# Performance work log

Hardware: AMD Instinct MI355X
Metric: run time of the kernel (lower is better)

## Reference

```python
import jax, jax.numpy as jnp
import numpy as np

D_MODEL = 128
NUM_HEADS = 8
DEPTH = D_MODEL // NUM_HEADS
NEG = -1e9


def _dense_params(key, d_in, d_out):
    kw, kb = jax.random.split(key)
    # Glorot-uniform like keras Dense default
    lim = np.sqrt(6.0 / (d_in + d_out))
    w = jax.random.uniform(kw, (d_in, d_out), jnp.float32, -lim, lim)
    b = jnp.zeros((d_out,), jnp.float32)
    return w, b


def setup_inputs() -> dict:
    key = jax.random.key(0)
    ks = jax.random.split(key, 16)
    B, N, M, d = 256, 128, 128, D_MODEL
    inp = {
        'x_self': jax.random.normal(ks[0], (B, N, d), jnp.float32),
        'adj_self': jax.random.randint(ks[1], (B, N, N), 0, 2, jnp.int32),
        'mask_self': jnp.ones((B, N), jnp.int32),
        'x_cross': jax.random.normal(ks[2], (B, M, d), jnp.float32),
        'mask_cross': jnp.ones((B, M), jnp.int32),
    }
    names = ['wq_s', 'wk_s', 'wv_s', 'wo_s', 'wq_c', 'wk_c', 'wv_c', 'wo_c']
    for i, nm in enumerate(names):
        w, b = _dense_params(ks[3 + i], d, d)
        inp[nm] = w
        inp['b' + nm[1:]] = b
    wg, bg = _dense_params(ks[12], 3 * d, d)
    inp['wg'] = wg
    inp['bg'] = bg
    return inp


def _split_heads(x):
    B, N, _ = x.shape
    return x.reshape(B, N, NUM_HEADS, DEPTH).transpose(0, 2, 1, 3)  # [B,H,N,depth]


def _merge_heads(x):
    B, H, N, Dp = x.shape
    return x.transpose(0, 2, 1, 3).reshape(B, N, H * Dp)


def _attention(q, k, v, mask, adj=None):
    # q,k,v: [B,H,Nq,depth]; mask: [B,Nk]; adj: [B,Nq,Nk] or None
    logits = jnp.einsum('bhqd,bhkd->bhqk', q, k) / jnp.sqrt(jnp.float32(DEPTH))
    if adj is not None:
        logits = logits + ((1.0 - adj.astype(jnp.float32)) * NEG)[:, None, :, :]
    logits = logits + ((1.0 - mask.astype(jnp.float32)) * NEG)[:, None, None, :]
    w = jax.nn.softmax(logits, axis=-1)
    return jnp.einsum('bhqk,bhkd->bhqd', w, v)


def reference(x_self, adj_self, mask_self, x_cross, mask_cross,
              wq_s, bq_s, wk_s, bk_s, wv_s, bv_s, wo_s, bo_s,
              wq_c, bq_c, wk_c, bk_c, wv_c, bv_c, wo_c, bo_c,
              wg, bg):
    # Self attention (adjacency + padding mask)
    q_s = _split_heads(x_self @ wq_s + bq_s)
    k_s = _split_heads(x_self @ wk_s + bk_s)
    v_s = _split_heads(x_self @ wv_s + bv_s)
    out_s = _merge_heads(_attention(q_s, k_s, v_s, mask_self, adj_self)) @ wo_s + bo_s
    # Cross attention (padding mask only); dropout inactive at inference
    q_c = _split_heads(x_self @ wq_c + bq_c)
    k_c = _split_heads(x_cross @ wk_c + bk_c)
    v_c = _split_heads(x_cross @ wv_c + bv_c)
    out_c = _merge_heads(_attention(q_c, k_c, v_c, mask_cross)) @ wo_c + bo_c
    # Sigmoid gate fusion
    gate = jax.nn.sigmoid(jnp.concatenate([x_self, out_s, out_c], axis=-1) @ wg + bg)
    return (1.0 - gate) * out_s + gate * out_c
```

## Files before the change

kernel.cpp:

```cpp
#include <hip/hip_runtime.h>
#include <hip/hip_bf16.h>

typedef _Float16 f16_t;
typedef __attribute__((ext_vector_type(8))) _Float16 f16x8;
typedef __attribute__((ext_vector_type(4))) float f32x4;

__device__ __forceinline__ f16x8 cvt8(const float* p) {
  float4 v0 = *(const float4*)p;
  float4 v1 = *(const float4*)(p + 4);
  f16x8 a;
  a[0] = (f16_t)v0.x; a[1] = (f16_t)v0.y; a[2] = (f16_t)v0.z; a[3] = (f16_t)v0.w;
  a[4] = (f16_t)v1.x; a[5] = (f16_t)v1.y; a[6] = (f16_t)v1.z; a[7] = (f16_t)v1.w;
  return a;
}

__global__ __launch_bounds__(256) void prep_kernel(
    const float* wq_s, const float* wk_s, const float* wv_s,
    const float* wq_c, const float* wk_c, const float* wv_c,
    const float* wo_s, const float* wo_c, const float* wg,
    const float* bos, const float* boc, const float* bgin,
    f16_t* WT, float* bgp)
{
  const int b = blockIdx.x;
  const int tid = threadIdx.x;
  if (b < 11) {
    __shared__ float t[128][129];
    const float* src; f16_t* dst; int ostride;
    switch (b) {
      case 0: src = wq_s; break; case 1: src = wk_s; break;
      case 2: src = wv_s; break; case 3: src = wq_c; break;
      case 4: src = wk_c; break; case 5: src = wv_c; break;
      case 6: src = wo_s; break; case 7: src = wo_c; break;
      default: src = wg + (size_t)(b - 8) * 16384; break;
    }
    if (b < 8) { dst = WT + (size_t)b * 16384; ostride = 128; }
    else       { dst = WT + 8 * 16384 + (b - 8) * 128; ostride = 384; }
#pragma unroll
    for (int i = 0; i < 64; ++i) {
      const int idx = tid + i * 256;
      t[idx & 127][idx >> 7] = src[idx];
    }
    __syncthreads();
#pragma unroll
    for (int i = 0; i < 64; ++i) {
      const int idx = tid + i * 256;
      const int c = idx >> 7, r = idx & 127;
      dst[(size_t)c * ostride + r] = (f16_t)t[c][r];
    }
  } else if (b < 13) {
    const int matsel = b - 11;
    const float* wo = matsel ? wo_c : wo_s;
    const int joff = 128 + matsel * 128;
    f16_t* dst = WT + (size_t)(11 + matsel) * 16384;
    const int wv = tid >> 6, ln = tid & 63, l15 = ln & 15, g = ln >> 4;
    f32x4 acc[2][8];
#pragma unroll
    for (int mm = 0; mm < 2; ++mm)
#pragma unroll
      for (int nt = 0; nt < 8; ++nt) acc[mm][nt] = (f32x4){0.f, 0.f, 0.f, 0.f};
#pragma unroll
    for (int kt = 0; kt < 4; ++kt) {
      f16x8 a[2];
#pragma unroll
      for (int mm = 0; mm < 2; ++mm) {
        const int crow = wv * 32 + mm * 16 + l15;
#pragma unroll
        for (int jj = 0; jj < 8; ++jj)
          a[mm][jj] = (f16_t)wg[(size_t)(joff + kt * 32 + g * 8 + jj) * 128 + crow];
      }
#pragma unroll
      for (int nt = 0; nt < 8; ++nt) {
        f16x8 bf = cvt8(wo + (size_t)(nt * 16 + l15) * 128 + kt * 32 + g * 8);
        acc[0][nt] = __builtin_amdgcn_mfma_f32_16x16x32_f16(a[0], bf, acc[0][nt], 0, 0, 0);
        acc[1][nt] = __builtin_amdgcn_mfma_f32_16x16x32_f16(a[1], bf, acc[1][nt], 0, 0, 0);
      }
    }
#pragma unroll
    for (int mm = 0; mm < 2; ++mm)
#pragma unroll
      for (int nt = 0; nt < 8; ++nt)
#pragma unroll
        for (int r = 0; r < 4; ++r) {
          const int c = wv * 32 + mm * 16 + g * 4 + r;
          dst[(size_t)c * 128 + nt * 16 + l15] = (f16_t)acc[mm][nt][r];
        }
  } else {
    if (tid < 128) {
      float acc = bgin[tid];
      for (int j = 0; j < 128; ++j)
        acc += bos[j] * wg[(size_t)(128 + j) * 128 + tid] +
               boc[j] * wg[(size_t)(256 + j) * 128 + tid];
      bgp[tid] = acc;
    }
  }
}

template <bool TRANSP>
__device__ __forceinline__ void gemm_w(
    const f16x8 afr[4], const f16_t* __restrict__ W, const float* __restrict__ bias,
    char* Ob, int l15, int g, int wv)
{
  f32x4 acc[8];
#pragma unroll
  for (int nt = 0; nt < 8; ++nt) acc[nt] = (f32x4){0.f, 0.f, 0.f, 0.f};
#pragma unroll
  for (int nt = 0; nt < 8; ++nt)
#pragma unroll
    for (int kt = 0; kt < 4; ++kt) {
      f16x8 b = *(const f16x8*)(W + (size_t)(nt * 16 + l15) * 128 + kt * 32 + g * 8);
      acc[nt] = __builtin_amdgcn_mfma_f32_16x16x32_f16(afr[kt], b, acc[nt], 0, 0, 0);
    }
#pragma unroll
  for (int nt = 0; nt < 8; ++nt) {
    const int col = nt * 16 + l15;
    const float bv = bias[col];
#pragma unroll
    for (int r = 0; r < 4; ++r) {
      const int row = wv * 16 + g * 4 + r;
      const f16_t v = (f16_t)(acc[nt][r] + bv);
      if (TRANSP)
        *(f16_t*)(Ob + col * 256 + ((row * 2) ^ ((col & 7) << 4))) = v;
      else
        *(f16_t*)(Ob + row * 256 + ((col * 2) ^ ((row & 7) << 4))) = v;
    }
  }
}

__device__ __forceinline__ void attn_wave(
    char* Qb, const char* Kb, const char* Vtb, const unsigned aw[4],
    char* Pw, int l15, int g, int wv)
{
  const int q = wv * 16 + l15;
  const int qsw = (q & 7) << 4;
  const int psw = (l15 & 7) << 4;
  const f32x4 zero = (f32x4){0.f, 0.f, 0.f, 0.f};

#pragma unroll
  for (int h = 0; h < 8; ++h) {
    f16x8 bq = {0, 0, 0, 0, 0, 0, 0, 0};
    if (g < 2) bq = *(const f16x8*)(Qb + q * 256 + ((h * 32 + g * 16) ^ qsw));
    f32x4 st[8];
#pragma unroll
    for (int kt = 0; kt < 8; ++kt) {
      const int krow = kt * 16 + l15;
      f16x8 ak = {0, 0, 0, 0, 0, 0, 0, 0};
      if (g < 2)
        ak = *(const f16x8*)(Kb + krow * 256 + ((h * 32 + g * 16) ^ ((krow & 7) << 4)));
      st[kt] = __builtin_amdgcn_mfma_f32_16x16x32_f16(ak, bq, zero, 0, 0, 0);
    }
    float psum = 0.f;
#pragma unroll
    for (int kt = 0; kt < 8; ++kt)
#pragma unroll
      for (int r = 0; r < 4; ++r) {
        const int k = kt * 16 + g * 4 + r;
        const float e = __expf(st[kt][r] * 0.25f - 8.f);
        const float p = ((aw[kt >> 1] >> (k & 31)) & 1u) ? e : 0.f;
        psum += p;
        st[kt][r] = p;
      }
    psum += __shfl_xor(psum, 16);
    psum += __shfl_xor(psum, 32);
    const float inv = 1.f / psum;

    f32x4 o = zero;
#pragma unroll
    for (int half = 0; half < 2; ++half) {
#pragma unroll
      for (int kt2 = 0; kt2 < 4; ++kt2) {
        const int kt = half * 4 + kt2;
        union { f16_t hh[4]; unsigned long long u; } pk;
#pragma unroll
        for (int r = 0; r < 4; ++r) pk.hh[r] = (f16_t)(st[kt][r] * inv);
        *(unsigned long long*)(Pw + l15 * 128 + ((kt2 * 32 + g * 8) ^ psw)) = pk.u;
      }
#pragma unroll
      for (int kt32 = 0; kt32 < 2; ++kt32) {
        f16x8 pa = *(const f16x8*)(Pw + l15 * 128 + ((kt32 * 64 + g * 16) ^ psw));
        const int d = h * 16 + l15;
        f16x8 vb = *(const f16x8*)(Vtb + d * 256 +
                     (((half * 64 + kt32 * 32 + g * 8) * 2) ^ ((d & 7) << 4)));
        o = __builtin_amdgcn_mfma_f32_16x16x32_f16(pa, vb, o, 0, 0, 0);
      }
    }
#pragma unroll
    for (int r = 0; r < 4; ++r) {
      const int qo = wv * 16 + g * 4 + r;
      *(f16_t*)(Qb + qo * 256 + (((h * 16 + l15) * 2) ^ ((qo & 7) << 4))) = (f16_t)o[r];
    }
  }
}

__global__ __launch_bounds__(512, 2) void fused_kernel(
    const float* __restrict__ Xs_g, const float* __restrict__ Xc_g,
    const int* __restrict__ adj, const int* __restrict__ mask_s,
    const int* __restrict__ mask_c, const f16_t* __restrict__ WT,
    const float* __restrict__ bq_s, const float* __restrict__ bk_s,
    const float* __restrict__ bv_s, const float* __restrict__ bq_c,
    const float* __restrict__ bk_c, const float* __restrict__ bv_c,
    const float* __restrict__ bos, const float* __restrict__ boc,
    const float* __restrict__ bgp, float* __restrict__ OUT)
{
  __shared__ __align__(16) char B0[32768];
  __shared__ __align__(16) char B1[32768];
  __shared__ __align__(16) char B2[32768];
  __shared__ __align__(16) char B3[32768];
  __shared__ __align__(16) char PR[16384];
  __shared__ unsigned mw_s[4], mwc_s[4];

  const int bb = blockIdx.x;
  const int tid = threadIdx.x;
  const int wv = tid >> 6, ln = tid & 63, l15 = ln & 15, g = ln >> 4;

  {
    const int r = tid >> 2, c0 = (tid & 3) * 32;
    const float* src = Xs_g + (size_t)bb * 16384 + r * 128 + c0;
    const int sw = (r & 7) << 4;
#pragma unroll
    for (int i = 0; i < 4; ++i) {
      f16x8 v = cvt8(src + i * 8);
      *(f16x8*)(B3 + r * 256 + ((c0 * 2 + i * 16) ^ sw)) = v;
    }
    const int4* ap = (const int4*)(adj + (size_t)bb * 16384 + r * 128 + (tid & 3) * 32);
    unsigned bits = 0;
#pragma unroll
    for (int i = 0; i < 8; ++i) {
      int4 a = ap[i];
      bits |= ((a.x != 0 ? 1u : 0u) | (a.y != 0 ? 2u : 0u) |
               (a.z != 0 ? 4u : 0u) | (a.w != 0 ? 8u : 0u)) << (i * 4);
    }
    *(unsigned*)(PR + r * 16 + (tid & 3) * 4) = bits;
  }
  if (tid < 128) {
    unsigned long long bm = __ballot(mask_s[bb * 128 + tid] != 0);
    if ((tid & 63) == 0) {
      mw_s[(tid >> 6) * 2 + 0] = (unsigned)bm;
      mw_s[(tid >> 6) * 2 + 1] = (unsigned)(bm >> 32);
    }
  } else if (tid < 256) {
    const int t = tid - 128;
    unsigned long long bm = __ballot(mask_c[bb * 128 + t] != 0);
    if ((t & 63) == 0) {
      mwc_s[(t >> 6) * 2 + 0] = (unsigned)bm;
      mwc_s[(t >> 6) * 2 + 1] = (unsigned)(bm >> 32);
    }
  }
  __syncthreads();

  {
    const int arow = wv * 16 + l15;
    const int asw = (arow & 7) << 4;
    f16x8 afr[4];
#pragma unroll
    for (int kt = 0; kt < 4; ++kt)
      afr[kt] = *(const f16x8*)(B3 + arow * 256 + ((kt * 64 + g * 16) ^ asw));
    gemm_w<false>(afr, WT + 0 * 16384, bq_s, B0, l15, g, wv);
    gemm_w<false>(afr, WT + 1 * 16384, bk_s, B1, l15, g, wv);
    gemm_w<true >(afr, WT + 2 * 16384, bv_s, B2, l15, g, wv);
    gemm_w<false>(afr, WT + 3 * 16384, bq_c, B3, l15, g, wv);
  }
  __syncthreads();

  {
    const int q_own = wv * 16 + l15;
    const uint4 a4 = *(const uint4*)(PR + q_own * 16);
    unsigned aw[4] = {a4.x & mw_s[0], a4.y & mw_s[1], a4.z & mw_s[2], a4.w & mw_s[3]};
    __syncthreads();
    attn_wave(B0, B1, B2, aw, PR + wv * 2048, l15, g, wv);
  }
  __syncthreads();

  {
    const int arow = wv * 16 + l15;
    f16x8 afr[4];
#pragma unroll
    for (int kt = 0; kt < 4; ++kt)
      afr[kt] = cvt8(Xc_g + (size_t)bb * 16384 + arow * 128 + kt * 32 + g * 8);
    gemm_w<false>(afr, WT + 4 * 16384, bk_c, B1, l15, g, wv);
    gemm_w<true >(afr, WT + 5 * 16384, bv_c, B2, l15, g, wv);
  }
  __syncthreads();

  {
    unsigned awc[4] = {mwc_s[0], mwc_s[1], mwc_s[2], mwc_s[3]};
    attn_wave(B3, B1, B2, awc, PR + wv * 2048, l15, g, wv);
  }
  __syncthreads();

  {
    const int arow = wv * 16 + l15;
    const int asw = (arow & 7) << 4;
    f16x8 aS[4], aC[4], aX[4];
#pragma unroll
    for (int kt = 0; kt < 4; ++kt) {
      aS[kt] = *(const f16x8*)(B0 + arow * 256 + ((kt * 64 + g * 16) ^ asw));
      aC[kt] = *(const f16x8*)(B3 + arow * 256 + ((kt * 64 + g * 16) ^ asw));
      aX[kt] = cvt8(Xs_g + (size_t)bb * 16384 + arow * 128 + kt * 32 + g * 8);
    }
    const f16_t* WoS = WT + 6 * 16384;
    const f16_t* WoC = WT + 7 * 16384;
    const f16_t* Wg1 = WT + 8 * 16384;
    const f16_t* W2p = WT + 11 * 16384;
    const f16_t* W3p = WT + 12 * 16384;
    f32x4 accS[8], accC[8], accG[8];
#pragma unroll
    for (int nt = 0; nt < 8; ++nt) {
      accS[nt] = (f32x4){0.f, 0.f, 0.f, 0.f};
      accC[nt] = (f32x4){0.f, 0.f, 0.f, 0.f};
      accG[nt] = (f32x4){0.f, 0.f, 0.f, 0.f};
    }
#pragma unroll
    for (int nt = 0; nt < 8; ++nt) {
      const size_t col = nt * 16 + l15;
#pragma unroll
      for (int kt = 0; kt < 4; ++kt) {
        const size_t ko = kt * 32 + g * 8;
        f16x8 bS = *(const f16x8*)(WoS + col * 128 + ko);
        f16x8 bC = *(const f16x8*)(WoC + col * 128 + ko);
        f16x8 bG = *(const f16x8*)(Wg1 + col * 384 + ko);
        f16x8 b2 = *(const f16x8*)(W2p + col * 128 + ko);
        f16x8 b3 = *(const f16x8*)(W3p + col * 128 + ko);
        accS[nt] = __builtin_amdgcn_mfma_f32_16x16x32_f16(aS[kt], bS, accS[nt], 0, 0, 0);
        accC[nt] = __builtin_amdgcn_mfma_f32_16x16x32_f16(aC[kt], bC, accC[nt], 0, 0, 0);
        accG[nt] = __builtin_amdgcn_mfma_f32_16x16x32_f16(aX[kt], bG, accG[nt], 0, 0, 0);
        accG[nt] = __builtin_amdgcn_mfma_f32_16x16x32_f16(aS[kt], b2, accG[nt], 0, 0, 0);
        accG[nt] = __builtin_amdgcn_mfma_f32_16x16x32_f16(aC[kt], b3, accG[nt], 0, 0, 0);
      }
    }
#pragma unroll
    for (int nt = 0; nt < 8; ++nt) {
      const int col = nt * 16 + l15;
      const float bS = bos[col], bC = boc[col], bG = bgp[col];
#pragma unroll
      for (int r = 0; r < 4; ++r) {
        const int row = wv * 16 + g * 4 + r;
        const float os = accS[nt][r] + bS;
        const float oc = accC[nt][r] + bC;
        const float gv = 1.f / (1.f + __expf(-(accG[nt][r] + bG)));
        OUT[(size_t)bb * 16384 + row * 128 + col] = (1.f - gv) * os + gv * oc;
      }
    }
  }
}

extern "C" void kernel_launch(void* const* d_in, const int* in_sizes, int n_in,
                              void* d_out, int out_size, void* d_ws, size_t ws_size,
                              hipStream_t stream)
{
  const float* x_self  = (const float*)d_in[0];
  const int*   adj     = (const int*)d_in[1];
  const int*   mask_s  = (const int*)d_in[2];
  const float* x_cross = (const float*)d_in[3];
  const int*   mask_c  = (const int*)d_in[4];
  const float* wq_s = (const float*)d_in[5];
  const float* bq_s = (const float*)d_in[6];
  const float* wk_s = (const float*)d_in[7];
  const float* bk_s = (const float*)d_in[8];
  const float* wv_s = (const float*)d_in[9];
  const float* bv_s = (const float*)d_in[10];
  const float* wo_s = (const float*)d_in[11];
  const float* bo_s = (const float*)d_in[12];
  const float* wq_c = (const float*)d_in[13];
  const float* bq_c = (const float*)d_in[14];
  const float* wk_c = (const float*)d_in[15];
  const float* bk_c = (const float*)d_in[16];
  const float* wv_c = (const float*)d_in[17];
  const float* bv_c = (const float*)d_in[18];
  const float* wo_c = (const float*)d_in[19];
  const float* bo_c = (const float*)d_in[20];
  const float* wg   = (const float*)d_in[21];
  const float* bg   = (const float*)d_in[22];
  float* out = (float*)d_out;

  f16_t* WT  = (f16_t*)d_ws;
  float* bgp = (float*)(WT + 13 * 16384);

  prep_kernel<<<14, 256, 0, stream>>>(wq_s, wk_s, wv_s, wq_c, wk_c, wv_c,
                                      wo_s, wo_c, wg, bo_s, bo_c, bg, WT, bgp);
  fused_kernel<<<256, 512, 0, stream>>>(x_self, x_cross, adj, mask_s, mask_c, WT,
                                        bq_s, bk_s, bv_s, bq_c, bk_c, bv_c,
                                        bo_s, bo_c, bgp, out);
}
```

Baseline: 132.8 us.

## Split fused attention block across 16 waves by row group and head half

The block grows from 512 to 1024 threads. Each of 16 waves owns a 16-row group and half of the output columns or heads, so per-wave accumulator counts are halved and more waves cover latency. The self and cross Q projections are kept in registers through a small per-wave scratch instead of full shared-memory Q buffers. The X tile is read straight from global memory rather than staged in LDS, and one barrier in the self-attention phase is removed. In exchange, launch_bounds(1024,4) caps registers per thread, the 160KB of LDS still allows only one block per CU, and each wave reloads the A fragments for its half of the columns.

New measurement: 143.1 us. 7.7% more time.

```diff
diff --git a/kernel.cpp b/kernel.cpp
--- a/kernel.cpp
+++ b/kernel.cpp
@@ -96,27 +96,27 @@
 }
 
 template <bool TRANSP>
-__device__ __forceinline__ void gemm_w(
+__device__ __forceinline__ void gemm4(
     const f16x8 afr[4], const f16_t* __restrict__ W, const float* __restrict__ bias,
-    char* Ob, int l15, int g, int wv)
-{
-  f32x4 acc[8];
-#pragma unroll
-  for (int nt = 0; nt < 8; ++nt) acc[nt] = (f32x4){0.f, 0.f, 0.f, 0.f};
-#pragma unroll
-  for (int nt = 0; nt < 8; ++nt)
+    char* Ob, int l15, int g, int rg, int colbase)
+{
+  f32x4 acc[4];
+#pragma unroll
+  for (int nt = 0; nt < 4; ++nt) acc[nt] = (f32x4){0.f, 0.f, 0.f, 0.f};
+#pragma unroll
+  for (int nt = 0; nt < 4; ++nt)
 #pragma unroll
     for (int kt = 0; kt < 4; ++kt) {
-      f16x8 b = *(const f16x8*)(W + (size_t)(nt * 16 + l15) * 128 + kt * 32 + g * 8);
+      f16x8 b = *(const f16x8*)(W + (size_t)(colbase + nt * 16 + l15) * 128 + kt * 32 + g * 8);
       acc[nt] = __builtin_amdgcn_mfma_f32_16x16x32_f16(afr[kt], b, acc[nt], 0, 0, 0);
     }
 #pragma unroll
-  for (int nt = 0; nt < 8; ++nt) {
-    const int col = nt * 16 + l15;
+  for (int nt = 0; nt < 4; ++nt) {
+    const int col = colbase + nt * 16 + l15;
     const float bv = bias[col];
 #pragma unroll
     for (int r = 0; r < 4; ++r) {
-      const int row = wv * 16 + g * 4 + r;
+      const int row = rg * 16 + g * 4 + r;
       const f16_t v = (f16_t)(acc[nt][r] + bv);
       if (TRANSP)
         *(f16_t*)(Ob + col * 256 + ((row * 2) ^ ((col & 7) << 4))) = v;
@@ -126,27 +126,58 @@
   }
 }
 
-__device__ __forceinline__ void attn_wave(
-    char* Qb, const char* Kb, const char* Vtb, const unsigned aw[4],
-    char* Pw, int l15, int g, int wv)
-{
-  const int q = wv * 16 + l15;
-  const int qsw = (q & 7) << 4;
-  const int psw = (l15 & 7) << 4;
+__device__ __forceinline__ void gemmQ(
+    const f16x8 afr[4], const f16_t* __restrict__ W, const float* __restrict__ bias,
+    char* scr, int l15, int g, int colbase, f16x8 bq[4])
+{
+  f32x4 acc[4];
+#pragma unroll
+  for (int nt = 0; nt < 4; ++nt) acc[nt] = (f32x4){0.f, 0.f, 0.f, 0.f};
+#pragma unroll
+  for (int nt = 0; nt < 4; ++nt)
+#pragma unroll
+    for (int kt = 0; kt < 4; ++kt) {
+      f16x8 b = *(const f16x8*)(W + (size_t)(colbase + nt * 16 + l15) * 128 + kt * 32 + g * 8);
+      acc[nt] = __builtin_amdgcn_mfma_f32_16x16x32_f16(afr[kt], b, acc[nt], 0, 0, 0);
+    }
+#pragma unroll
+  for (int nt = 0; nt < 4; ++nt) {
+    const int col = colbase + nt * 16 + l15;
+    const float bv = bias[col];
+    const int dloc = nt * 16 + l15;
+#pragma unroll
+    for (int r = 0; r < 4; ++r) {
+      const int qp = g * 4 + r;
+      *(f16_t*)(scr + qp * 128 + ((dloc * 2) ^ ((qp & 7) << 4))) = (f16_t)(acc[nt][r] + bv);
+    }
+  }
+#pragma unroll
+  for (int h = 0; h < 4; ++h) {
+    f16x8 z = {0, 0, 0, 0, 0, 0, 0, 0};
+    bq[h] = (g < 2)
+      ? *(const f16x8*)(scr + l15 * 128 + (((h * 16 + g * 8) * 2) ^ ((l15 & 7) << 4)))
+      : z;
+  }
+}
+
+__device__ __forceinline__ void attn_w(
+    const char* Kb, const char* Vtb, char* ATTo, char* Pw,
+    const f16x8 bq[4], const unsigned aw[4],
+    int l15, int g, int rg, int ch)
+{
   const f32x4 zero = (f32x4){0.f, 0.f, 0.f, 0.f};
-
-#pragma unroll
-  for (int h = 0; h < 8; ++h) {
-    f16x8 bq = {0, 0, 0, 0, 0, 0, 0, 0};
-    if (g < 2) bq = *(const f16x8*)(Qb + q * 256 + ((h * 32 + g * 16) ^ qsw));
+  const int psw = (l15 & 3) << 4;
+#pragma unroll
+  for (int hp = 0; hp < 4; ++hp) {
+    const int h = ch * 4 + hp;
     f32x4 st[8];
 #pragma unroll
     for (int kt = 0; kt < 8; ++kt) {
       const int krow = kt * 16 + l15;
       f16x8 ak = {0, 0, 0, 0, 0, 0, 0, 0};
       if (g < 2)
-        ak = *(const f16x8*)(Kb + krow * 256 + ((h * 32 + g * 16) ^ ((krow & 7) << 4)));
-      st[kt] = __builtin_amdgcn_mfma_f32_16x16x32_f16(ak, bq, zero, 0, 0, 0);
+        ak = *(const f16x8*)(Kb + krow * 256 + (((h * 16 + g * 8) * 2) ^ ((krow & 7) << 4)));
+      st[kt] = __builtin_amdgcn_mfma_f32_16x16x32_f16(ak, bq[hp], zero, 0, 0, 0);
     }
     float psum = 0.f;
 #pragma unroll
@@ -155,9 +186,9 @@
       for (int r = 0; r < 4; ++r) {
         const int k = kt * 16 + g * 4 + r;
         const float e = __expf(st[kt][r] * 0.25f - 8.f);
-        const float p = ((aw[kt >> 1] >> (k & 31)) & 1u) ? e : 0.f;
+        const float p = ((aw[k >> 5] >> (k & 31)) & 1u) ? e : 0.f;
+        st[kt][r] = p;
         psum += p;
-        st[kt][r] = p;
       }
     psum += __shfl_xor(psum, 16);
     psum += __shfl_xor(psum, 32);
@@ -165,33 +196,29 @@
 
     f32x4 o = zero;
 #pragma unroll
-    for (int half = 0; half < 2; ++half) {
-#pragma unroll
-      for (int kt2 = 0; kt2 < 4; ++kt2) {
-        const int kt = half * 4 + kt2;
+    for (int qt = 0; qt < 4; ++qt) {
+#pragma unroll
+      for (int hf = 0; hf < 2; ++hf) {
+        const int kt = qt * 2 + hf;
         union { f16_t hh[4]; unsigned long long u; } pk;
 #pragma unroll
         for (int r = 0; r < 4; ++r) pk.hh[r] = (f16_t)(st[kt][r] * inv);
-        *(unsigned long long*)(Pw + l15 * 128 + ((kt2 * 32 + g * 8) ^ psw)) = pk.u;
-      }
-#pragma unroll
-      for (int kt32 = 0; kt32 < 2; ++kt32) {
-        f16x8 pa = *(const f16x8*)(Pw + l15 * 128 + ((kt32 * 64 + g * 16) ^ psw));
-        const int d = h * 16 + l15;
-        f16x8 vb = *(const f16x8*)(Vtb + d * 256 +
-                     (((half * 64 + kt32 * 32 + g * 8) * 2) ^ ((d & 7) << 4)));
-        o = __builtin_amdgcn_mfma_f32_16x16x32_f16(pa, vb, o, 0, 0, 0);
-      }
+        *(unsigned long long*)(Pw + l15 * 64 + (((hf * 16 + g * 4) * 2) ^ psw)) = pk.u;
+      }
+      f16x8 pa = *(const f16x8*)(Pw + l15 * 64 + ((g * 16) ^ psw));
+      const int d = h * 16 + l15;
+      f16x8 vb = *(const f16x8*)(Vtb + d * 256 + (((qt * 32 + g * 8) * 2) ^ ((d & 7) << 4)));
+      o = __builtin_amdgcn_mfma_f32_16x16x32_f16(pa, vb, o, 0, 0, 0);
     }
 #pragma unroll
     for (int r = 0; r < 4; ++r) {
-      const int qo = wv * 16 + g * 4 + r;
-      *(f16_t*)(Qb + qo * 256 + (((h * 16 + l15) * 2) ^ ((qo & 7) << 4))) = (f16_t)o[r];
-    }
-  }
-}
-
-__global__ __launch_bounds__(512, 2) void fused_kernel(
+      const int row = rg * 16 + g * 4 + r;
+      *(f16_t*)(ATTo + row * 256 + (((h * 16 + l15) * 2) ^ ((row & 7) << 4))) = (f16_t)o[r];
+    }
+  }
+}
+
+__global__ __launch_bounds__(1024, 4) void fused2_kernel(
     const float* __restrict__ Xs_g, const float* __restrict__ Xc_g,
     const int* __restrict__ adj, const int* __restrict__ mask_s,
     const int* __restrict__ mask_c, const f16_t* __restrict__ WT,
@@ -201,27 +228,23 @@
     const float* __restrict__ bos, const float* __restrict__ boc,
     const float* __restrict__ bgp, float* __restrict__ OUT)
 {
-  __shared__ __align__(16) char B0[32768];
-  __shared__ __align__(16) char B1[32768];
-  __shared__ __align__(16) char B2[32768];
-  __shared__ __align__(16) char B3[32768];
+  __shared__ __align__(16) char Kb[32768];
+  __shared__ __align__(16) char Vtb[32768];
+  __shared__ __align__(16) char ATTs[32768];
+  __shared__ __align__(16) char ATTc[32768];
   __shared__ __align__(16) char PR[16384];
-  __shared__ unsigned mw_s[4], mwc_s[4];
+  __shared__ unsigned mwS[4], mwC[4];
 
   const int bb = blockIdx.x;
   const int tid = threadIdx.x;
   const int wv = tid >> 6, ln = tid & 63, l15 = ln & 15, g = ln >> 4;
-
-  {
-    const int r = tid >> 2, c0 = (tid & 3) * 32;
-    const float* src = Xs_g + (size_t)bb * 16384 + r * 128 + c0;
-    const int sw = (r & 7) << 4;
-#pragma unroll
-    for (int i = 0; i < 4; ++i) {
-      f16x8 v = cvt8(src + i * 8);
-      *(f16x8*)(B3 + r * 256 + ((c0 * 2 + i * 16) ^ sw)) = v;
-    }
-    const int4* ap = (const int4*)(adj + (size_t)bb * 16384 + r * 128 + (tid & 3) * 32);
+  const int rg = wv & 7, ch = wv >> 3;
+  const int colbase = ch * 64;
+  const int arow = rg * 16 + l15;
+
+  if (tid < 512) {
+    const int r = tid >> 2, w = tid & 3;
+    const int4* ap = (const int4*)(adj + (size_t)bb * 16384 + r * 128 + w * 32);
     unsigned bits = 0;
 #pragma unroll
     for (int i = 0; i < 8; ++i) {
@@ -229,72 +252,60 @@
       bits |= ((a.x != 0 ? 1u : 0u) | (a.y != 0 ? 2u : 0u) |
                (a.z != 0 ? 4u : 0u) | (a.w != 0 ? 8u : 0u)) << (i * 4);
     }
-    *(unsigned*)(PR + r * 16 + (tid & 3) * 4) = bits;
-  }
-  if (tid < 128) {
-    unsigned long long bm = __ballot(mask_s[bb * 128 + tid] != 0);
-    if ((tid & 63) == 0) {
-      mw_s[(tid >> 6) * 2 + 0] = (unsigned)bm;
-      mw_s[(tid >> 6) * 2 + 1] = (unsigned)(bm >> 32);
-    }
-  } else if (tid < 256) {
-    const int t = tid - 128;
-    unsigned long long bm = __ballot(mask_c[bb * 128 + t] != 0);
-    if ((t & 63) == 0) {
-      mwc_s[(t >> 6) * 2 + 0] = (unsigned)bm;
-      mwc_s[(t >> 6) * 2 + 1] = (unsigned)(bm >> 32);
-    }
+    *(unsigned*)(ATTc + r * 16 + w * 4) = bits;
+  }
+  if (wv < 2) {
+    unsigned long long bm = __ballot(mask_s[bb * 128 + wv * 64 + ln] != 0);
+    if (ln == 0) { mwS[wv * 2] = (unsigned)bm; mwS[wv * 2 + 1] = (unsigned)(bm >> 32); }
+  } else if (wv < 4) {
+    unsigned long long bm = __ballot(mask_c[bb * 128 + (wv - 2) * 64 + ln] != 0);
+    if (ln == 0) { mwC[(wv - 2) * 2] = (unsigned)bm; mwC[(wv - 2) * 2 + 1] = (unsigned)(bm >> 32); }
+  }
+
+  f16x8 bqs[4], bqc[4];
+  {
+    f16x8 afr[4];
+#pragma unroll
+    for (int kt = 0; kt < 4; ++kt)
+      afr[kt] = cvt8(Xs_g + (size_t)bb * 16384 + arow * 128 + kt * 32 + g * 8);
+    gemm4<false>(afr, WT + 1 * 16384, bk_s, Kb, l15, g, rg, colbase);
+    gemm4<true >(afr, WT + 2 * 16384, bv_s, Vtb, l15, g, rg, colbase);
+    char* scr = ATTs + wv * 2048;
+    gemmQ(afr, WT + 0 * 16384, bq_s, scr, l15, g, colbase, bqs);
+    gemmQ(afr, WT + 3 * 16384, bq_c, scr, l15, g, colbase, bqc);
   }
   __syncthreads();
 
   {
-    const int arow = wv * 16 + l15;
-    const int asw = (arow & 7) << 4;
-    f16x8 afr[4];
-#pragma unroll
-    for (int kt = 0; kt < 4; ++kt)
-      afr[kt] = *(const f16x8*)(B3 + arow * 256 + ((kt * 64 + g * 16) ^ asw));
-    gemm_w<false>(afr, WT + 0 * 16384, bq_s, B0, l15, g, wv);
-    gemm_w<false>(afr, WT + 1 * 16384, bk_s, B1, l15, g, wv);
-    gemm_w<true >(afr, WT + 2 * 16384, bv_s, B2, l15, g, wv);
-    gemm_w<false>(afr, WT + 3 * 16384, bq_c, B3, l15, g, wv);
+    const uint4 a4 = *(const uint4*)(ATTc + arow * 16);
+    unsigned aw[4] = {a4.x & mwS[0], a4.y & mwS[1], a4.z & mwS[2], a4.w & mwS[3]};
+    attn_w(Kb, Vtb, ATTs, PR + wv * 1024, bqs, aw, l15, g, rg, ch);
   }
   __syncthreads();
 
   {
-    const int q_own = wv * 16 + l15;
-    const uint4 a4 = *(const uint4*)(PR + q_own * 16);
-    unsigned aw[4] = {a4.x & mw_s[0], a4.y & mw_s[1], a4.z & mw_s[2], a4.w & mw_s[3]};
-    __syncthreads();
-    attn_wave(B0, B1, B2, aw, PR + wv * 2048, l15, g, wv);
-  }
-  __syncthreads();
-
-  {
-    const int arow = wv * 16 + l15;
     f16x8 afr[4];
 #pragma unroll
     for (int kt = 0; kt < 4; ++kt)
       afr[kt] = cvt8(Xc_g + (size_t)bb * 16384 + arow * 128 + kt * 32 + g * 8);
-    gemm_w<false>(afr, WT + 4 * 16384, bk_c, B1, l15, g, wv);
-    gemm_w<true >(afr, WT + 5 * 16384, bv_c, B2, l15, g, wv);
+    gemm4<false>(afr, WT + 4 * 16384, bk_c, Kb, l15, g, rg, colbase);
+    gemm4<true >(afr, WT + 5 * 16384, bv_c, Vtb, l15, g, rg, colbase);
   }
   __syncthreads();
 
   {
-    unsigned awc[4] = {mwc_s[0], mwc_s[1], mwc_s[2], mwc_s[3]};
-    attn_wave(B3, B1, B2, awc, PR + wv * 2048, l15, g, wv);
+    unsigned aw[4] = {mwC[0], mwC[1], mwC[2], mwC[3]};
+    attn_w(Kb, Vtb, ATTc, PR + wv * 1024, bqc, aw, l15, g, rg, ch);
   }
   __syncthreads();
 
   {
-    const int arow = wv * 16 + l15;
     const int asw = (arow & 7) << 4;
     f16x8 aS[4], aC[4], aX[4];
 #pragma unroll
     for (int kt = 0; kt < 4; ++kt) {
-      aS[kt] = *(const f16x8*)(B0 + arow * 256 + ((kt * 64 + g * 16) ^ asw));
-      aC[kt] = *(const f16x8*)(B3 + arow * 256 + ((kt * 64 + g * 16) ^ asw));
+      aS[kt] = *(const f16x8*)(ATTs + arow * 256 + ((kt * 64 + g * 16) ^ asw));
+      aC[kt] = *(const f16x8*)(ATTc + arow * 256 + ((kt * 64 + g * 16) ^ asw));
       aX[kt] = cvt8(Xs_g + (size_t)bb * 16384 + arow * 128 + kt * 32 + g * 8);
     }
     const f16_t* WoS = WT + 6 * 16384;
@@ -302,16 +313,16 @@
     const f16_t* Wg1 = WT + 8 * 16384;
     const f16_t* W2p = WT + 11 * 16384;
     const f16_t* W3p = WT + 12 * 16384;
-    f32x4 accS[8], accC[8], accG[8];
-#pragma unroll
-    for (int nt = 0; nt < 8; ++nt) {
+    f32x4 accS[4], accC[4], accG[4];
+#pragma unroll
+    for (int nt = 0; nt < 4; ++nt) {
       accS[nt] = (f32x4){0.f, 0.f, 0.f, 0.f};
       accC[nt] = (f32x4){0.f, 0.f, 0.f, 0.f};
       accG[nt] = (f32x4){0.f, 0.f, 0.f, 0.f};
     }
 #pragma unroll
-    for (int nt = 0; nt < 8; ++nt) {
-      const size_t col = nt * 16 + l15;
+    for (int nt = 0; nt < 4; ++nt) {
+      const size_t col = colbase + nt * 16 + l15;
 #pragma unroll
       for (int kt = 0; kt < 4; ++kt) {
         const size_t ko = kt * 32 + g * 8;
@@ -328,12 +339,12 @@
       }
     }
 #pragma unroll
-    for (int nt = 0; nt < 8; ++nt) {
-      const int col = nt * 16 + l15;
+    for (int nt = 0; nt < 4; ++nt) {
+      const int col = colbase + nt * 16 + l15;
       const float bS = bos[col], bC = boc[col], bG = bgp[col];
 #pragma unroll
       for (int r = 0; r < 4; ++r) {
-        const int row = wv * 16 + g * 4 + r;
+        const int row = rg * 16 + g * 4 + r;
         const float os = accS[nt][r] + bS;
         const float oc = accC[nt][r] + bC;
         const float gv = 1.f / (1.f + __expf(-(accG[nt][r] + bG)));
@@ -377,7 +388,7 @@
 
   prep_kernel<<<14, 256, 0, stream>>>(wq_s, wk_s, wv_s, wq_c, wk_c, wv_c,
                                       wo_s, wo_c, wg, bo_s, bo_c, bg, WT, bgp);
-  fused_kernel<<<256, 512, 0, stream>>>(x_self, x_cross, adj, mask_s, mask_c, WT,
-                                        bq_s, bk_s, bv_s, bq_c, bk_c, bv_c,
-                                        bo_s, bo_c, bgp, out);
-}
+  fused2_kernel<<<256, 1024, 0, stream>>>(x_self, x_cross, adj, mask_s, mask_c, WT,
+                                          bq_s, bk_s, bv_s, bq_c, bk_c, bv_c,
+                                          bo_s, bo_c, bgp, out);
+}
```
